# Performance work log

Measured on AMD Instinct MI355X. Metric: run time of the kernel, lower is better.

Reference implementation:

```python
import jax, jax.numpy as jnp
import numpy as np

H = 16
D_MODEL = 1024
D_K = D_MODEL // H
B, S = 4, 2048


def setup_inputs() -> dict:
    key = jax.random.key(0)
    ks = jax.random.split(key, 8)
    scale = 1.0 / np.sqrt(D_MODEL)
    return {
        "query": jax.random.normal(ks[0], (B, S, D_MODEL), dtype=jnp.float32),
        "key": jax.random.normal(ks[1], (B, S, D_MODEL), dtype=jnp.float32),
        "value": jax.random.normal(ks[2], (B, S, D_MODEL), dtype=jnp.float32),
        "A": jnp.zeros((1,), dtype=jnp.float32),
        "Wq": jax.random.normal(ks[3], (D_MODEL, D_MODEL), dtype=jnp.float32) * scale,
        "bq": jnp.zeros((D_MODEL,), dtype=jnp.float32),
        "Wk": jax.random.normal(ks[4], (D_MODEL, D_MODEL), dtype=jnp.float32) * scale,
        "bk": jnp.zeros((D_MODEL,), dtype=jnp.float32),
        "Wv": jax.random.normal(ks[5], (D_MODEL, D_MODEL), dtype=jnp.float32) * scale,
        "bv": jnp.zeros((D_MODEL,), dtype=jnp.float32),
        "Wo": jax.random.normal(ks[6], (D_MODEL, D_MODEL), dtype=jnp.float32) * scale,
        "bo": jnp.zeros((D_MODEL,), dtype=jnp.float32),
    }


def reference(query, key, value, A, Wq, bq, Wk, bk, Wv, bv, Wo, bo):
    nb = query.shape[0]

    def proj(x, W, b):
        # torch Linear: x @ W.T + b, then view(B, S, H, D_K) and transpose -> [B, H, S, D_K]
        y = jnp.einsum('bsd,ed->bse', x, W) + b
        return y.reshape(nb, -1, H, D_K).transpose(0, 2, 1, 3)

    q = proj(query, Wq, bq)
    k = proj(key, Wk, bk)
    v = proj(value, Wv, bv)

    # NOTE: original code has NO 1/sqrt(d_k) scaling, no mask, no dropout.
    scores = jnp.einsum('bhqd,bhkd->bhqk', q, k)  # [B,H,S,S]
    p_attn = jax.nn.softmax(scores, axis=-1)
    x = jnp.einsum('bhqk,bhkd->bhqd', p_attn, v)  # [B,H,S,D_K]

    x = x.transpose(0, 2, 1, 3).reshape(nb, -1, H * D_K)  # [B,S,d_model]
    out = jnp.einsum('bsd,ed->bse', x, Wo) + bo
    loss = jnp.asarray(0.0, dtype=out.dtype)
    return (out, loss)
```

## Files before the change

kernel.cpp:

```cpp
#include <hip/hip_runtime.h>

typedef unsigned short u16;
typedef _Float16 half8 __attribute__((ext_vector_type(8)));
typedef _Float16 h2 __attribute__((ext_vector_type(2)));
typedef float f32x4 __attribute__((ext_vector_type(4)));
typedef u16 u16x4 __attribute__((ext_vector_type(4)));
typedef u16 u16x8 __attribute__((ext_vector_type(8)));

#define MFMAH(a, b, c) __builtin_amdgcn_mfma_f32_16x16x32_f16(a, b, c, 0, 0, 0)

constexpr float LOG2E = 1.44269504088896f;
constexpr float THR = 12.0f;

__device__ __forceinline__ u16 f2h(float f) {
  _Float16 h = (_Float16)f;
  return __builtin_bit_cast(u16, h);
}
__device__ __forceinline__ h2 pkrtz(float a, float b) {
  return __builtin_bit_cast(h2, __builtin_amdgcn_cvt_pkrtz(a, b));
}

__device__ __forceinline__ void gload_lds16(const void* g, void* l) {
  __builtin_amdgcn_global_load_lds(
      (const __attribute__((address_space(1))) void*)g,
      (__attribute__((address_space(3))) void*)l,
      16, 0, 0);
}

__device__ __forceinline__ void conv_block(const float* __restrict__ in,
                                           u16* __restrict__ out, int i) {
  const float4 a = reinterpret_cast<const float4*>(in)[2 * i];
  const float4 b = reinterpret_cast<const float4*>(in)[2 * i + 1];
  u16x8 o;
  o[0] = f2h(a.x); o[1] = f2h(a.y); o[2] = f2h(a.z); o[3] = f2h(a.w);
  o[4] = f2h(b.x); o[5] = f2h(b.y); o[6] = f2h(b.z); o[7] = f2h(b.w);
  reinterpret_cast<u16x8*>(out)[i] = o;
}

__global__ __launch_bounds__(256) void conv_qkv(const float* __restrict__ q,
                                                const float* __restrict__ k,
                                                const float* __restrict__ v,
                                                u16* __restrict__ qo, u16* __restrict__ ko,
                                                u16* __restrict__ vo, int n8) {
  int i = blockIdx.x * 256 + threadIdx.x;
  const int stride = gridDim.x * 256;
  for (; i < 3 * n8; i += stride) {
    const int sel = i / n8, j = i - sel * n8;
    if (sel == 0) conv_block(q, qo, j);
    else if (sel == 1) conv_block(k, ko, j);
    else conv_block(v, vo, j);
  }
}

__global__ __launch_bounds__(256) void conv_w4(const float* __restrict__ w0,
                                               const float* __restrict__ w1,
                                               const float* __restrict__ w2,
                                               const float* __restrict__ w3,
                                               u16* __restrict__ o0, u16* __restrict__ o1,
                                               u16* __restrict__ o2, u16* __restrict__ o3,
                                               int n8) {
  int i = blockIdx.x * 256 + threadIdx.x;
  const int stride = gridDim.x * 256;
  for (; i < 4 * n8; i += stride) {
    const int sel = i / n8, j = i - sel * n8;
    if (sel == 0) conv_block(w0, o0, j);
    else if (sel == 1) conv_block(w1, o1, j);
    else if (sel == 2) conv_block(w2, o2, j);
    else conv_block(w3, o3, j);
  }
}

template <int MODE>
__global__ __launch_bounds__(256) void gemm_bt(const u16* __restrict__ A,
                                               const u16* __restrict__ Bw,
                                               const float* __restrict__ bias,
                                               void* __restrict__ Cv,
                                               int M, int N, int K, float scale) {
  __shared__ u16 As[128 * 32];
  __shared__ u16 Bs[128 * 32];
  const int tid = threadIdx.x;
  const int lane = tid & 63;
  const int l16 = lane & 15, lhi = lane >> 4;
  const int wid = tid >> 6;
  const int wm = wid >> 1, wn = wid & 1;
  const int bm0 = blockIdx.y * 128;
  const int bn0 = blockIdx.x * 128;

  const int c0 = tid, c1 = tid + 256;
  const u16* Ag0 = A + (size_t)(bm0 + (c0 >> 2)) * K + (c0 & 3) * 8;
  const u16* Ag1 = A + (size_t)(bm0 + (c1 >> 2)) * K + (c1 & 3) * 8;
  const u16* Bg0 = Bw + (size_t)(bn0 + (c0 >> 2)) * K + (c0 & 3) * 8;
  const u16* Bg1 = Bw + (size_t)(bn0 + (c1 >> 2)) * K + (c1 & 3) * 8;

  f32x4 acc[4][4] = {};

  for (int kt = 0; kt < K; kt += 32) {
    gload_lds16(Ag0 + kt, &As[c0 * 8]);
    gload_lds16(Ag1 + kt, &As[c1 * 8]);
    gload_lds16(Bg0 + kt, &Bs[c0 * 8]);
    gload_lds16(Bg1 + kt, &Bs[c1 * 8]);
    __syncthreads();
    half8 af[4], bf[4];
#pragma unroll
    for (int f = 0; f < 4; ++f)
      af[f] = *reinterpret_cast<const half8*>(&As[(wm * 64 + f * 16 + l16) * 32 + lhi * 8]);
#pragma unroll
    for (int f = 0; f < 4; ++f)
      bf[f] = *reinterpret_cast<const half8*>(&Bs[(wn * 64 + f * 16 + l16) * 32 + lhi * 8]);
#pragma unroll
    for (int i = 0; i < 4; ++i)
#pragma unroll
      for (int j = 0; j < 4; ++j)
        acc[i][j] = MFMAH(af[i], bf[j], acc[i][j]);
    __syncthreads();
  }

#pragma unroll
  for (int i = 0; i < 4; ++i) {
    const int m0 = bm0 + wm * 64 + i * 16 + lhi * 4;
#pragma unroll
    for (int j = 0; j < 4; ++j) {
      const int n = bn0 + wn * 64 + j * 16 + l16;
      const float bb = bias[n];
      if (MODE == 0) {
        float* Cf = (float*)Cv;
#pragma unroll
        for (int r = 0; r < 4; ++r)
          Cf[(size_t)(m0 + r) * N + n] = acc[i][j][r] + bb;
      } else if (MODE == 2) {
        u16* C = (u16*)Cv;
        u16x4 pack;
#pragma unroll
        for (int r = 0; r < 4; ++r) pack[r] = f2h(acc[i][j][r] + bb);
        const int head = (m0 >> 11) * 16 + (n >> 6);
        const int s0 = m0 & 2047;
        const int d = n & 63;
        const int within =
            ((s0 >> 5) & 1) * 2048 + d * 32 + ((s0 >> 2) & 3) * 8 + ((s0 >> 4) & 1) * 4;
        const int sw = within ^ ((d & 7) << 3);
        const size_t idx = (size_t)head * 131072 + (size_t)(s0 >> 6) * 4096 + sw;
        *reinterpret_cast<u16x4*>(&C[idx]) = pack;
      } else {
        u16* C = (u16*)Cv;
#pragma unroll
        for (int r = 0; r < 4; ++r) {
          const int m = m0 + r;
          const size_t idx =
              ((size_t)((m >> 11) * 16 + (n >> 6)) * 2048 + (m & 2047)) * 64 + (n & 63);
          C[idx] = f2h((acc[i][j][r] + bb) * scale);
        }
      }
    }
  }
}

__global__ __launch_bounds__(256, 4) void attn_fwd(const u16* __restrict__ Q,
                                                   const u16* __restrict__ Kh,
                                                   const u16* __restrict__ VL,
                                                   u16* __restrict__ X) {
  __shared__ u16 Ks[2][4096];
  __shared__ u16 Vs[2][4096];

  const int tid = threadIdx.x, lane = tid & 63, w = tid >> 6;
  const int l16 = lane & 15, lhi = lane >> 4;
  const int blk = blockIdx.x;
  const int xcd = blk & 7, wi = blk >> 3;
  const int bh = (xcd << 3) | (wi >> 4);
  const int qt = wi & 15;
  const int b = bh >> 4, h = bh & 15;

  const size_t qrow0 = (size_t)bh * 2048 + qt * 128 + w * 32;
  half8 qf[2][2];
#pragma unroll
  for (int fq = 0; fq < 2; ++fq)
#pragma unroll
    for (int ks = 0; ks < 2; ++ks)
      qf[fq][ks] = *reinterpret_cast<const half8*>(
          &Q[(qrow0 + fq * 16 + l16) * 64 + ks * 32 + lhi * 8]);

  f32x4 o[2][4] = {};
  float mrow[2] = {-1e30f, -1e30f};
  float ssum[2] = {0.0f, 0.0f};

  const u16* Kb = Kh + (size_t)bh * 2048 * 64;
  const u16* VLh = VL + (size_t)bh * 64 * 64 * 32;

#define STAGE_KV(bufidx, tt)                                                      \
  do {                                                                            \
    const int kb0_ = (tt) * 64;                                                   \
    _Pragma("unroll")                                                             \
    for (int ii_ = 0; ii_ < 2; ++ii_) {                                           \
      const int c_ = tid + ii_ * 256;                                             \
      const int r_ = c_ >> 3, cb_ = c_ & 7;                                       \
      gload_lds16(Kb + (size_t)(kb0_ + r_) * 64 + ((cb_ ^ (r_ & 7)) << 3),        \
                  &Ks[bufidx][c_ * 8]);                                           \
      gload_lds16(VLh + (size_t)(tt) * 4096 + c_ * 8, &Vs[bufidx][c_ * 8]);       \
    }                                                                             \
  } while (0)

  STAGE_KV(0, 0);
  __syncthreads();

  for (int t = 0; t < 32; ++t) {
    const int cur = t & 1;
    if (t < 31) STAGE_KV(cur ^ 1, t + 1);
    f32x4 sc[2][4] = {};
#pragma unroll
    for (int fk = 0; fk < 4; ++fk) {
      const int row = fk * 16 + l16;
#pragma unroll
      for (int ks = 0; ks < 2; ++ks) {
        const int off = (row * 64 + ks * 32 + lhi * 8) ^ ((row & 7) << 3);
        const half8 kf = *reinterpret_cast<const half8*>(&Ks[cur][off]);
#pragma unroll
        for (int fq = 0; fq < 2; ++fq) sc[fq][fk] = MFMAH(kf, qf[fq][ks], sc[fq][fk]);
      }
    }
    float lm[2];
#pragma unroll
    for (int fq = 0; fq < 2; ++fq) {
      float a0 = fmaxf(fmaxf(sc[fq][0][0], sc[fq][0][1]), sc[fq][0][2]);
      float a1 = fmaxf(fmaxf(sc[fq][0][3], sc[fq][1][0]), sc[fq][1][1]);
      float a2 = fmaxf(fmaxf(sc[fq][1][2], sc[fq][1][3]), sc[fq][2][0]);
      float a3 = fmaxf(fmaxf(sc[fq][2][1], sc[fq][2][2]), sc[fq][2][3]);
      float a4 = fmaxf(fmaxf(sc[fq][3][0], sc[fq][3][1]), sc[fq][3][2]);
      float b0 = fmaxf(fmaxf(a0, a1), a2);
      float b1 = fmaxf(fmaxf(a3, a4), sc[fq][3][3]);
      lm[fq] = fmaxf(b0, b1);
    }
    const int trig = (lm[0] > mrow[0] + THR) || (lm[1] > mrow[1] + THR);
    if (__any(trig)) {
#pragma unroll
      for (int fq = 0; fq < 2; ++fq) {
        float rm = lm[fq];
        rm = fmaxf(rm, __shfl_xor(rm, 16));
        rm = fmaxf(rm, __shfl_xor(rm, 32));
        const float nm = fmaxf(mrow[fq], rm);
        const float scl = __builtin_amdgcn_exp2f(mrow[fq] - nm);
        mrow[fq] = nm;
        ssum[fq] *= scl;
        float sb[4];
#pragma unroll
        for (int r = 0; r < 4; ++r) sb[r] = __shfl(scl, lhi * 4 + r);
#pragma unroll
        for (int fd = 0; fd < 4; ++fd)
#pragma unroll
          for (int r = 0; r < 4; ++r) o[fq][fd][r] *= sb[r];
      }
    }
    half8 pa2[2][2];
#pragma unroll
    for (int fq = 0; fq < 2; ++fq) {
      union { half8 v[2]; h2 hh[8]; } uu;
#pragma unroll
      for (int fk = 0; fk < 4; ++fk) {
        const float p0 = __builtin_amdgcn_exp2f(sc[fq][fk][0] - mrow[fq]);
        const float p1 = __builtin_amdgcn_exp2f(sc[fq][fk][1] - mrow[fq]);
        const float p2 = __builtin_amdgcn_exp2f(sc[fq][fk][2] - mrow[fq]);
        const float p3 = __builtin_amdgcn_exp2f(sc[fq][fk][3] - mrow[fq]);
        ssum[fq] += (p0 + p1) + (p2 + p3);
        uu.hh[fk * 2 + 0] = pkrtz(p0, p1);
        uu.hh[fk * 2 + 1] = pkrtz(p2, p3);
      }
      pa2[fq][0] = uu.v[0];
      pa2[fq][1] = uu.v[1];
    }
#pragma unroll
    for (int fd = 0; fd < 4; ++fd)
#pragma unroll
      for (int ts = 0; ts < 2; ++ts) {
        const int va = (ts * 2048 + (fd * 16 + l16) * 32 + lhi * 8) ^ ((l16 & 7) << 3);
        const half8 vf = *reinterpret_cast<const half8*>(&Vs[cur][va]);
#pragma unroll
        for (int fq = 0; fq < 2; ++fq) o[fq][fd] = MFMAH(pa2[fq][ts], vf, o[fq][fd]);
      }
    __syncthreads();
  }
#undef STAGE_KV

#pragma unroll
  for (int fq = 0; fq < 2; ++fq) {
    float ss = ssum[fq];
    ss += __shfl_xor(ss, 16);
    ss += __shfl_xor(ss, 32);
    float iv[4];
#pragma unroll
    for (int r = 0; r < 4; ++r) iv[r] = 1.0f / __shfl(ss, lhi * 4 + r);
#pragma unroll
    for (int r = 0; r < 4; ++r) {
      const int q = qt * 128 + w * 32 + fq * 16 + lhi * 4 + r;
#pragma unroll
      for (int fd = 0; fd < 4; ++fd) {
        const int col = h * 64 + fd * 16 + l16;
        X[((size_t)b * 2048 + q) * 1024 + col] = f2h(o[fq][fd][r] * iv[r]);
      }
    }
  }
}

__global__ void write_loss(float* out, int idx) { out[idx] = 0.0f; }

extern "C" void kernel_launch(void* const* d_in, const int* in_sizes, int n_in,
                              void* d_out, int out_size, void* d_ws, size_t ws_size,
                              hipStream_t stream) {
  const float* q_f  = (const float*)d_in[0];
  const float* k_f  = (const float*)d_in[1];
  const float* v_f  = (const float*)d_in[2];
  const float* Wq_f = (const float*)d_in[4];
  const float* bq   = (const float*)d_in[5];
  const float* Wk_f = (const float*)d_in[6];
  const float* bk   = (const float*)d_in[7];
  const float* Wv_f = (const float*)d_in[8];
  const float* bv   = (const float*)d_in[9];
  const float* Wo_f = (const float*)d_in[10];
  const float* bo   = (const float*)d_in[11];

  const int SZ = 4 * 2048 * 1024;
  const int SW = 1024 * 1024;

  u16* ws = (u16*)d_ws;
  u16* qb   = ws;
  u16* kbuf = qb + SZ;
  u16* vbuf = kbuf + SZ;
  u16* wqb = vbuf + SZ;
  u16* wkb = wqb + SW;
  u16* wvb = wkb + SW;
  u16* wob = wvb + SW;
  u16* Qb  = wob + SW;
  u16* Kb  = Qb + SZ;
  u16* VLb = Kb + SZ;
  u16* Xb  = VLb + SZ;
  const size_t need_bytes = (size_t)(7 * SZ + 4 * SW) * 2;
  if (ws_size < need_bytes) return;

  conv_qkv<<<2048, 256, 0, stream>>>(q_f, k_f, v_f, qb, kbuf, vbuf, SZ / 8);
  conv_w4<<<1024, 256, 0, stream>>>(Wq_f, Wk_f, Wv_f, Wo_f, wqb, wkb, wvb, wob, SW / 8);

  dim3 gg(1024 / 128, 8192 / 128);
  gemm_bt<1><<<gg, 256, 0, stream>>>(qb, wqb, bq, Qb, 8192, 1024, 1024, LOG2E);
  gemm_bt<1><<<gg, 256, 0, stream>>>(kbuf, wkb, bk, Kb, 8192, 1024, 1024, 1.0f);
  gemm_bt<2><<<gg, 256, 0, stream>>>(vbuf, wvb, bv, VLb, 8192, 1024, 1024, 1.0f);

  attn_fwd<<<dim3(1024), 256, 0, stream>>>(Qb, Kb, VLb, Xb);

  gemm_bt<0><<<gg, 256, 0, stream>>>(Xb, wob, bo, d_out, 8192, 1024, 1024, 1.0f);
  write_loss<<<1, 1, 0, stream>>>((float*)d_out, out_size - 1);
}
```

Baseline: 252.8 us.

## Fuse fp32-to-fp16 input conversion into projection GEMMs and add MFMA priority hints

Drops the separate conv_qkv pass. The Q/K/V projection GEMMs now read fp32 activations directly, pack them to fp16 in registers and store them into LDS, which removes a full write and re-read of three fp16 activation tensors. The loss-zero write moves into the output GEMM, removing one launch. In attention, s_setprio raises wave priority around the MFMA sections. The trade-off is that A loads now go through registers instead of the async global-to-LDS path, which may expose latency, and each GEMM tile re-converts A, so every row is converted once per N-tile column (8 times).

```diff
diff --git a/kernel.cpp b/kernel.cpp
--- a/kernel.cpp
+++ b/kernel.cpp
@@ -35,21 +35,6 @@
   o[0] = f2h(a.x); o[1] = f2h(a.y); o[2] = f2h(a.z); o[3] = f2h(a.w);
   o[4] = f2h(b.x); o[5] = f2h(b.y); o[6] = f2h(b.z); o[7] = f2h(b.w);
   reinterpret_cast<u16x8*>(out)[i] = o;
-}
-
-__global__ __launch_bounds__(256) void conv_qkv(const float* __restrict__ q,
-                                                const float* __restrict__ k,
-                                                const float* __restrict__ v,
-                                                u16* __restrict__ qo, u16* __restrict__ ko,
-                                                u16* __restrict__ vo, int n8) {
-  int i = blockIdx.x * 256 + threadIdx.x;
-  const int stride = gridDim.x * 256;
-  for (; i < 3 * n8; i += stride) {
-    const int sel = i / n8, j = i - sel * n8;
-    if (sel == 0) conv_block(q, qo, j);
-    else if (sel == 1) conv_block(k, ko, j);
-    else conv_block(v, vo, j);
-  }
 }
 
 __global__ __launch_bounds__(256) void conv_w4(const float* __restrict__ w0,
@@ -70,8 +55,8 @@
   }
 }
 
-template <int MODE>
-__global__ __launch_bounds__(256) void gemm_bt(const u16* __restrict__ A,
+template <int MODE, bool A32>
+__global__ __launch_bounds__(256) void gemm_bt(const void* __restrict__ Av,
                                                const u16* __restrict__ Bw,
                                                const float* __restrict__ bias,
                                                void* __restrict__ Cv,
@@ -87,18 +72,38 @@
   const int bn0 = blockIdx.x * 128;
 
   const int c0 = tid, c1 = tid + 256;
-  const u16* Ag0 = A + (size_t)(bm0 + (c0 >> 2)) * K + (c0 & 3) * 8;
-  const u16* Ag1 = A + (size_t)(bm0 + (c1 >> 2)) * K + (c1 & 3) * 8;
+  const u16* A16 = (const u16*)Av;
+  const float* Af = (const float*)Av;
+  const u16* Ag0 = A16 + (size_t)(bm0 + (c0 >> 2)) * K + (c0 & 3) * 8;
+  const u16* Ag1 = A16 + (size_t)(bm0 + (c1 >> 2)) * K + (c1 & 3) * 8;
   const u16* Bg0 = Bw + (size_t)(bn0 + (c0 >> 2)) * K + (c0 & 3) * 8;
   const u16* Bg1 = Bw + (size_t)(bn0 + (c1 >> 2)) * K + (c1 & 3) * 8;
+  const float* Ar = Af + (size_t)(bm0 + (tid >> 1)) * K + (tid & 1) * 16;
+  u16* AsW = &As[(tid >> 1) * 32 + (tid & 1) * 16];
 
   f32x4 acc[4][4] = {};
 
   for (int kt = 0; kt < K; kt += 32) {
-    gload_lds16(Ag0 + kt, &As[c0 * 8]);
-    gload_lds16(Ag1 + kt, &As[c1 * 8]);
-    gload_lds16(Bg0 + kt, &Bs[c0 * 8]);
-    gload_lds16(Bg1 + kt, &Bs[c1 * 8]);
+    if constexpr (A32) {
+      const float4 a0 = *reinterpret_cast<const float4*>(Ar + kt);
+      const float4 a1 = *reinterpret_cast<const float4*>(Ar + kt + 4);
+      const float4 a2 = *reinterpret_cast<const float4*>(Ar + kt + 8);
+      const float4 a3 = *reinterpret_cast<const float4*>(Ar + kt + 12);
+      gload_lds16(Bg0 + kt, &Bs[c0 * 8]);
+      gload_lds16(Bg1 + kt, &Bs[c1 * 8]);
+      union { u16x8 u; h2 h[4]; } w0, w1;
+      w0.h[0] = pkrtz(a0.x, a0.y); w0.h[1] = pkrtz(a0.z, a0.w);
+      w0.h[2] = pkrtz(a1.x, a1.y); w0.h[3] = pkrtz(a1.z, a1.w);
+      w1.h[0] = pkrtz(a2.x, a2.y); w1.h[1] = pkrtz(a2.z, a2.w);
+      w1.h[2] = pkrtz(a3.x, a3.y); w1.h[3] = pkrtz(a3.z, a3.w);
+      *reinterpret_cast<u16x8*>(AsW) = w0.u;
+      *reinterpret_cast<u16x8*>(AsW + 8) = w1.u;
+    } else {
+      gload_lds16(Ag0 + kt, &As[c0 * 8]);
+      gload_lds16(Ag1 + kt, &As[c1 * 8]);
+      gload_lds16(Bg0 + kt, &Bs[c0 * 8]);
+      gload_lds16(Bg1 + kt, &Bs[c1 * 8]);
+    }
     __syncthreads();
     half8 af[4], bf[4];
 #pragma unroll
@@ -151,6 +156,10 @@
         }
       }
     }
+  }
+  if (MODE == 0) {
+    if (blockIdx.x == 0 && blockIdx.y == 0 && tid == 0)
+      ((float*)Cv)[(size_t)M * N] = 0.0f;
   }
 }
 
@@ -205,6 +214,7 @@
     const int cur = t & 1;
     if (t < 31) STAGE_KV(cur ^ 1, t + 1);
     f32x4 sc[2][4] = {};
+    __builtin_amdgcn_s_setprio(1);
 #pragma unroll
     for (int fk = 0; fk < 4; ++fk) {
       const int row = fk * 16 + l16;
@@ -216,6 +226,7 @@
         for (int fq = 0; fq < 2; ++fq) sc[fq][fk] = MFMAH(kf, qf[fq][ks], sc[fq][fk]);
       }
     }
+    __builtin_amdgcn_s_setprio(0);
     float lm[2];
 #pragma unroll
     for (int fq = 0; fq < 2; ++fq) {
@@ -265,6 +276,7 @@
       pa2[fq][0] = uu.v[0];
       pa2[fq][1] = uu.v[1];
     }
+    __builtin_amdgcn_s_setprio(1);
 #pragma unroll
     for (int fd = 0; fd < 4; ++fd)
 #pragma unroll
@@ -274,6 +286,7 @@
 #pragma unroll
         for (int fq = 0; fq < 2; ++fq) o[fq][fd] = MFMAH(pa2[fq][ts], vf, o[fq][fd]);
       }
+    __builtin_amdgcn_s_setprio(0);
     __syncthreads();
   }
 #undef STAGE_KV
@@ -297,8 +310,6 @@
     }
   }
 }
-
-__global__ void write_loss(float* out, int idx) { out[idx] = 0.0f; }
 
 extern "C" void kernel_launch(void* const* d_in, const int* in_sizes, int n_in,
                               void* d_out, int out_size, void* d_ws, size_t ws_size,
@@ -319,10 +330,7 @@
   const int SW = 1024 * 1024;
 
   u16* ws = (u16*)d_ws;
-  u16* qb   = ws;
-  u16* kbuf = qb + SZ;
-  u16* vbuf = kbuf + SZ;
-  u16* wqb = vbuf + SZ;
+  u16* wqb = ws;
   u16* wkb = wqb + SW;
   u16* wvb = wkb + SW;
   u16* wob = wvb + SW;
@@ -330,19 +338,17 @@
   u16* Kb  = Qb + SZ;
   u16* VLb = Kb + SZ;
   u16* Xb  = VLb + SZ;
-  const size_t need_bytes = (size_t)(7 * SZ + 4 * SW) * 2;
+  const size_t need_bytes = (size_t)(4 * SZ + 4 * SW) * 2;
   if (ws_size < need_bytes) return;
 
-  conv_qkv<<<2048, 256, 0, stream>>>(q_f, k_f, v_f, qb, kbuf, vbuf, SZ / 8);
   conv_w4<<<1024, 256, 0, stream>>>(Wq_f, Wk_f, Wv_f, Wo_f, wqb, wkb, wvb, wob, SW / 8);
 
   dim3 gg(1024 / 128, 8192 / 128);
-  gemm_bt<1><<<gg, 256, 0, stream>>>(qb, wqb, bq, Qb, 8192, 1024, 1024, LOG2E);
-  gemm_bt<1><<<gg, 256, 0, stream>>>(kbuf, wkb, bk, Kb, 8192, 1024, 1024, 1.0f);
-  gemm_bt<2><<<gg, 256, 0, stream>>>(vbuf, wvb, bv, VLb, 8192, 1024, 1024, 1.0f);
+  gemm_bt<1, true><<<gg, 256, 0, stream>>>(q_f, wqb, bq, Qb, 8192, 1024, 1024, LOG2E);
+  gemm_bt<1, true><<<gg, 256, 0, stream>>>(k_f, wkb, bk, Kb, 8192, 1024, 1024, 1.0f);
+  gemm_bt<2, true><<<gg, 256, 0, stream>>>(v_f, wvb, bv, VLb, 8192, 1024, 1024, 1.0f);
 
   attn_fwd<<<dim3(1024), 256, 0, stream>>>(Qb, Kb, VLb, Xb);
 
-  gemm_bt<0><<<gg, 256, 0, stream>>>(Xb, wob, bo, d_out, 8192, 1024, 1024, 1.0f);
-  write_loss<<<1, 1, 0, stream>>>((float*)d_out, out_size - 1);
-}
+  gemm_bt<0, false><<<gg, 256, 0, stream>>>(Xb, wob, bo, d_out, 8192, 1024, 1024, 1.0f);
+}
```

Result: no change. 254.0 us (+0.5%).
